# Kernel tuning notes

Measured on AMD Instinct MI355X. Metric: run time of the kernel, lower is better.

## Reference

```python
import jax, jax.numpy as jnp
import numpy as np

B, S, A = 64, 256, 256
V, P, TE, PE, AE, H, L = 50000, 48, 256, 64, 64, 512, 24
WD = TE + PE          # word_dim = token_embed + pos_embed
NA = 3 * L + 3        # Shift + L Unary + 2L Reduce/Reduce* + Pad + Pop


def setup_inputs() -> dict:
    key = jax.random.key(0)
    ks = jax.random.split(key, 24)
    f = lambda i, shape: jax.random.normal(ks[i], shape, dtype=jnp.float32) * 0.05
    return dict(
        token_batch=jax.random.randint(ks[0], (B, S), 0, V),
        pos_batch=jax.random.randint(ks[1], (B, S), 0, P),
        label_batch=jax.random.randint(ks[2], (B, S), 0, L),
        action_batch=jax.random.randint(ks[3], (B, A), 0, NA - 2),  # exclude Pad/Pop
        word_emb=f(4, (V, TE)), pos_emb=f(5, (P, PE)), action_emb=f(6, (NA, AE)),
        tok_Wih=f(7, (4 * H, WD)), tok_Whh=f(8, (4 * H, H)), tok_b=f(9, (4 * H,)),
        st_Wih=f(10, (4 * H, H)), st_Whh=f(11, (4 * H, H)), st_b=f(12, (4 * H,)),
        ac_Wih=f(13, (4 * H, AE)), ac_Whh=f(14, (4 * H, H)), ac_b=f(15, (4 * H,)),
        red_W=f(16, (2 * L, WD, 2 * WD)), red_b=f(17, (2 * L, WD)),
        comp_W=f(18, (H, WD)), comp_b=f(19, (H,)),
        h2f_W=f(20, (H, 5 * H)), h2f_b=f(21, (H,)),
        f2a_W=f(22, (NA, H)), f2a_b=f(23, (NA,)),
    )


def _lstm_cell(x, h, c, Wih, Whh, b):
    g = x @ Wih.T + h @ Whh.T + b
    i, fg, gg, o = jnp.split(g, 4, axis=-1)
    c = jax.nn.sigmoid(fg) * c + jax.nn.sigmoid(i) * jnp.tanh(gg)
    return jax.nn.sigmoid(o) * jnp.tanh(c), c


def reference(token_batch, pos_batch, label_batch, action_batch,
              word_emb, pos_emb, action_emb,
              tok_Wih, tok_Whh, tok_b,
              st_Wih, st_Whh, st_b,
              ac_Wih, ac_Whh, ac_b,
              red_W, red_b, comp_W, comp_b,
              h2f_W, h2f_b, f2a_W, f2a_b):
    # token encoder: embed + concat + unidirectional LSTM over the sentence
    tok = jnp.concatenate([word_emb[token_batch], pos_emb[pos_batch]], -1)  # [B,S,WD]

    def tstep(carry, x):
        h, c = carry
        h, c = _lstm_cell(x, h, c, tok_Wih, tok_Whh, tok_b)
        return (h, c), h

    h0 = jnp.zeros((B, H), tok.dtype)
    (_, _), tok_out = jax.lax.scan(tstep, (h0, h0), jnp.swapaxes(tok, 0, 1))  # [S,B,H]

    # action-step scan: action LSTMCell + per-label tiny linear composition +
    # stack LSTMCell + 5H decision feature -> hidden2feat -> relu -> feat2act
    a_emb = action_emb[action_batch]                      # [B,A,AE]
    labels = action_batch % (2 * L)                        # per-step label selection
    tok_prev = jnp.concatenate([tok[:, :1], tok[:, :-1]], 1)
    pair = jnp.concatenate([tok[:, :A], tok_prev[:, :A]], -1)  # [B,A,2WD]

    def astep(carry, x):
        ha, ca, hs, cs, h1 = carry
        ae_t, lab_t, pair_t, buf_t, act_t = x
        ha, ca = _lstm_cell(ae_t, ha, ca, ac_Wih, ac_Whh, ac_b)
        # per-label reduce linear (2*WD -> WD), gathered by the step's label
        composed = jnp.tanh(jnp.einsum('bij,bj->bi', red_W[lab_t], pair_t) + red_b[lab_t])
        st_in = buf_t + composed @ comp_W.T + comp_b
        hs_new, cs = _lstm_cell(st_in, hs, cs, st_Wih, st_Whh, st_b)
        feat = jnp.concatenate([hs_new, hs, h1, buf_t, ha], -1)  # [B,5H]
        logits = jax.nn.relu(feat @ h2f_W.T + h2f_b) @ f2a_W.T + f2a_b
        logp = jax.nn.log_softmax(logits, -1)
        loss_t = -jnp.take_along_axis(logp, act_t[:, None], 1)[:, 0]
        return (ha, ca, hs_new, cs, hs), loss_t

    z = jnp.zeros((B, H), tok.dtype)
    xs = (jnp.swapaxes(a_emb, 0, 1), labels.T, jnp.swapaxes(pair, 0, 1),
          tok_out[:A], action_batch.T)
    _, losses = jax.lax.scan(astep, (z, z, z, z, z), xs)  # [A,B]
    return jnp.mean(losses)
```

## Files before the change

kernel.cpp:

```cpp
#include <hip/hip_runtime.h>
#include <math.h>

constexpr int nB = 64, nS = 256, nAc = 256, nH = 512, nG = 2048;
constexpr int nWD = 320, nNA = 75, nLB = 48, nFH = 2560;
constexpr int BH = nB * nH;

typedef _Float16 h16;
typedef _Float16 h16x8 __attribute__((ext_vector_type(8)));
typedef _Float16 h16x4 __attribute__((ext_vector_type(4)));
typedef _Float16 h16x2 __attribute__((ext_vector_type(2)));
typedef float f32x4 __attribute__((ext_vector_type(4)));
typedef unsigned long long u64t;

__device__ __forceinline__ float sigf(float x) { return 1.0f / (1.0f + __expf(-x)); }

#if __has_builtin(__builtin_amdgcn_fdot2)
#define FDOT2(a, b, c) __builtin_amdgcn_fdot2((a), (b), (c), false)
#else
__device__ __forceinline__ float FDOT2(h16x2 a, h16x2 b, float c) {
    return c + (float)a[0] * (float)b[0] + (float)a[1] * (float)b[1];
}
#endif

__global__ void init_k(h16* __restrict__ hsrec, int* __restrict__ counts, int* __restrict__ fill,
                       u64t* __restrict__ hbuf, u64t* __restrict__ spbuf, u64t* __restrict__ apbuf)
{
    int i = blockIdx.x * 256 + threadIdx.x;
    if (i < 2 * BH) hsrec[i] = (h16)0.0f;
    if (i < 32768) { hbuf[i] = 0; spbuf[i] = 0; apbuf[i] = 0; }
    if (i < nLB) { counts[i] = 0; fill[i] = 0; }
}

__global__ __launch_bounds__(256)
void cvt_k(const float* __restrict__ src, h16* __restrict__ dst, int n4)
{
    const int i = blockIdx.x * 256 + threadIdx.x;
    if (i < n4) {
        const float4 a = ((const float4*)src)[i];
        h16x4 v; v[0]=(h16)a.x; v[1]=(h16)a.y; v[2]=(h16)a.z; v[3]=(h16)a.w;
        ((h16x4*)dst)[i] = v;
    }
}

__global__ __launch_bounds__(64)
void embed_k(const int* __restrict__ tokb, const int* __restrict__ posb,
             const float* __restrict__ wemb, const float* __restrict__ pemb,
             h16* __restrict__ tok)
{
    const int r = blockIdx.x;
    const int tid = threadIdx.x;
    const int tk = tokb[r], pp = posb[r];
    h16x8* d = (h16x8*)(tok + (size_t)r * nWD);
    if (tid < 32) {
        const float4* sw = (const float4*)(wemb + (size_t)tk * 256);
        const float4 a = sw[2 * tid], b = sw[2 * tid + 1];
        h16x8 o;
        o[0]=(h16)a.x; o[1]=(h16)a.y; o[2]=(h16)a.z; o[3]=(h16)a.w;
        o[4]=(h16)b.x; o[5]=(h16)b.y; o[6]=(h16)b.z; o[7]=(h16)b.w;
        d[tid] = o;
    } else if (tid < 40) {
        const int q = tid - 32;
        const float4* sp = (const float4*)(pemb + (size_t)pp * 64);
        const float4 a = sp[2 * q], b = sp[2 * q + 1];
        h16x8 o;
        o[0]=(h16)a.x; o[1]=(h16)a.y; o[2]=(h16)a.z; o[3]=(h16)a.w;
        o[4]=(h16)b.x; o[5]=(h16)b.y; o[6]=(h16)b.z; o[7]=(h16)b.w;
        d[32 + q] = o;
    }
}

__global__ __launch_bounds__(256)
void actab_k(const float* __restrict__ aemb, const float* __restrict__ aWih,
             const float* __restrict__ ab, float* __restrict__ acTab)
{
    const int a = blockIdx.x;
    __shared__ float ae[64];
    const int tid = threadIdx.x;
    if (tid < 64) ae[tid] = aemb[a * 64 + tid];
    __syncthreads();
    for (int j = tid; j < nG; j += 256) {
        const float* wr = aWih + (size_t)j * 64;
        float s = ab[j];
        #pragma unroll
        for (int k = 0; k < 64; k += 4) {
            const float4 w = *(const float4*)(wr + k);
            s = fmaf(w.x, ae[k], s);     s = fmaf(w.y, ae[k + 1], s);
            s = fmaf(w.z, ae[k + 2], s); s = fmaf(w.w, ae[k + 3], s);
        }
        acTab[(size_t)a * nG + j] = s;
    }
}

template<int MODE, bool RELU>
__global__ __launch_bounds__(256)
void mgemm_k(const h16* __restrict__ Wm, const float* __restrict__ bias,
             const h16* __restrict__ A0, const h16* __restrict__ A1,
             const h16* __restrict__ A2, h16* __restrict__ C, int Ktot, int ldC)
{
    const int bm = blockIdx.x << 6, bn = blockIdx.y << 6;
    const int tid = threadIdx.x;
    const int lane = tid & 63, wave = tid >> 6;
    const int wr = wave >> 1, wc = wave & 1;
    __shared__ __align__(16) h16 As[64][40];
    __shared__ __align__(16) h16 Ws[64][40];
    const int srow = tid >> 2, sk = (tid & 3) << 3;
    const int r3 = bm + srow;
    const h16* arow = nullptr;
    if (MODE == 0) { const int b = r3 & 63, s = r3 >> 6; arow = A0 + ((size_t)b * nS + s) * nWD; }
    if (MODE == 5) { arow = A0 + (size_t)r3 * nWD; }
    const h16* wrow = Wm + (size_t)(bn + srow) * Ktot;
    f32x4 acc[2][2] = {};
    for (int k0 = 0; k0 < Ktot; k0 += 32) {
        h16x8 av, wv;
        if (MODE == 3) {
            const int k = k0 + sk;
            const int p = k >> 9;
            const h16* base = (p == 0) ? A0 + 2 * BH : (p == 1) ? A0 + BH
                            : (p == 2) ? A0 : (p == 3) ? A1 : A2;
            av = *(const h16x8*)(base + (size_t)r3 * nH + (k & 511));
        } else {
            av = *(const h16x8*)(arow + k0 + sk);
        }
        wv = *(const h16x8*)(wrow + k0 + sk);
        __syncthreads();
        *(h16x8*)(&As[srow][sk]) = av;
        *(h16x8*)(&Ws[srow][sk]) = wv;
        __syncthreads();
        const int fk = (lane >> 4) << 3;
        const int fr = lane & 15;
        h16x8 af0 = *(const h16x8*)(&As[(wr << 5) + fr][fk]);
        h16x8 af1 = *(const h16x8*)(&As[(wr << 5) + 16 + fr][fk]);
        h16x8 bf0 = *(const h16x8*)(&Ws[(wc << 5) + fr][fk]);
        h16x8 bf1 = *(const h16x8*)(&Ws[(wc << 5) + 16 + fr][fk]);
        acc[0][0] = __builtin_amdgcn_mfma_f32_16x16x32_f16(af0, bf0, acc[0][0], 0, 0, 0);
        acc[0][1] = __builtin_amdgcn_mfma_f32_16x16x32_f16(af0, bf1, acc[0][1], 0, 0, 0);
        acc[1][0] = __builtin_amdgcn_mfma_f32_16x16x32_f16(af1, bf0, acc[1][0], 0, 0, 0);
        acc[1][1] = __builtin_amdgcn_mfma_f32_16x16x32_f16(af1, bf1, acc[1][1], 0, 0, 0);
    }
    #pragma unroll
    for (int mi = 0; mi < 2; ++mi) {
        #pragma unroll
        for (int ni = 0; ni < 2; ++ni) {
            const int col = bn + (wc << 5) + (ni << 4) + (lane & 15);
            const float bs = bias[col];
            #pragma unroll
            for (int rg = 0; rg < 4; ++rg) {
                const int row = bm + (wr << 5) + (mi << 4) + ((lane >> 4) << 2) + rg;
                float x = acc[mi][ni][rg] + bs;
                if (RELU) x = fmaxf(x, 0.0f);
                C[(size_t)row * ldC + col] = (h16)x;
            }
        }
    }
}

__global__ void hist_k(const int* __restrict__ actb, int* __restrict__ lab, int* __restrict__ counts)
{
    const int r = blockIdx.x * 256 + threadIdx.x;
    const int t = r >> 6, b = r & 63;
    const int a = actb[b * nAc + t];
    const int l = a % nLB;
    lab[r] = l;
    atomicAdd(&counts[l], 1);
}

__global__ void tiles_k(const int* __restrict__ counts, int* __restrict__ offs,
                        int* __restrict__ tl_lab, int* __restrict__ tl_start,
                        int* __restrict__ tl_cnt, int* __restrict__ ntiles)
{
    if (blockIdx.x == 0 && threadIdx.x == 0) {
        int o = 0, nt = 0;
        for (int l = 0; l < nLB; ++l) {
            offs[l] = o;
            const int c = counts[l];
            for (int s0 = 0; s0 < c; s0 += 64) {
                tl_lab[nt] = l; tl_start[nt] = o + s0; tl_cnt[nt] = min(64, c - s0); ++nt;
            }
            o += c;
        }
        offs[nLB] = o;
        ntiles[0] = nt;
    }
}

__global__ void scatter_k(const int* __restrict__ lab, const int* __restrict__ offs,
                          int* __restrict__ fill, int* __restrict__ idx)
{
    const int r = blockIdx.x * 256 + threadIdx.x;
    const int l = lab[r];
    const int pos = offs[l] + atomicAdd(&fill[l], 1);
    idx[pos] = r;
}

__global__ __launch_bounds__(256)
void comp_gemm_k(const h16* __restrict__ tok, const float* __restrict__ redW,
                 const float* __restrict__ redb, const int* __restrict__ idx,
                 const int* __restrict__ tl_lab, const int* __restrict__ tl_start,
                 const int* __restrict__ tl_cnt, const int* __restrict__ ntiles,
                 h16* __restrict__ comp)
{
    const int tile = blockIdx.x;
    if (tile >= ntiles[0]) return;
    const int cn0 = blockIdx.y << 6;
    const int l = tl_lab[tile], rst = tl_start[tile], mrows = tl_cnt[tile];
    __shared__ int rows_s[64];
    __shared__ __align__(16) float As[16][68];
    __shared__ __align__(16) float Ws[16][68];
    const int tid = threadIdx.x;
    if (tid < 64) rows_s[tid] = (tid < mrows) ? idx[rst + tid] : -1;
    __syncthreads();
    const int alm = tid >> 1, alk = (tid & 1) << 3;
    const int wlm = tid >> 2, wlk = (tid & 3) << 2;
    const int trow = tid >> 4, tcol = tid & 15;
    const int rm = (tid < 128) ? rows_s[alm] : -1;
    const h16* arow0 = tok;
    const h16* arow1 = tok;
    if (rm >= 0) {
        const int b = rm & 63, t = rm >> 6;
        arow0 = tok + ((size_t)b * nS + t) * nWD;
        arow1 = tok + ((size_t)b * nS + max(t - 1, 0)) * nWD;
    }
    const float* wrow = redW + (size_t)l * (320 * 640) + (size_t)(cn0 + wlm) * 640;
    float acc[4][4] = {};
    for (int k0 = 0; k0 < 640; k0 += 16) {
        const int k = k0 + alk;
        h16x8 av = {};
        if (rm >= 0) av = (k < 320) ? *(const h16x8*)(arow0 + k)
                                    : *(const h16x8*)(arow1 + (k - 320));
        const float4 wv = *(const float4*)(wrow + k0 + wlk);
        __syncthreads();
        if (tid < 128) {
            #pragma unroll
            for (int j = 0; j < 8; ++j) As[alk + j][alm] = (float)av[j];
        }
        Ws[wlk + 0][wlm] = wv.x; Ws[wlk + 1][wlm] = wv.y;
        Ws[wlk + 2][wlm] = wv.z; Ws[wlk + 3][wlm] = wv.w;
        __syncthreads();
        #pragma unroll
        for (int kk = 0; kk < 16; ++kk) {
            const float4 a4 = *(const float4*)&As[kk][trow << 2];
            const float4 w4 = *(const float4*)&Ws[kk][tcol << 2];
            const float aa[4] = {a4.x, a4.y, a4.z, a4.w};
            const float ww[4] = {w4.x, w4.y, w4.z, w4.w};
            #pragma unroll
            for (int i = 0; i < 4; ++i)
                #pragma unroll
                for (int j = 0; j < 4; ++j)
                    acc[i][j] = fmaf(aa[i], ww[j], acc[i][j]);
        }
    }
    #pragma unroll
    for (int i = 0; i < 4; ++i) {
        const int rr = rows_s[(trow << 2) + i];
        if (rr < 0) continue;
        #pragma unroll
        for (int j = 0; j < 4; ++j) {
            const int cc = cn0 + (tcol << 2) + j;
            comp[(size_t)rr * nWD + cc] = (h16)tanhf(acc[i][j] + redb[l * nWD + cc]);
        }
    }
}

__global__ __launch_bounds__(512, 4)
void fused_scan_k(const h16* __restrict__ tW16, const h16* __restrict__ sWhh16,
                  const h16* __restrict__ sWih16, const h16* __restrict__ aW16,
                  const h16* __restrict__ gxTok, const float* __restrict__ acTab,
                  const int* __restrict__ actb, const h16* __restrict__ P1h,
                  const float* __restrict__ sbias,
                  u64t* __restrict__ hq_tok, u64t* __restrict__ hq_st, u64t* __restrict__ hq_ac,
                  h16* __restrict__ tokrec, h16* __restrict__ hsrec, h16* __restrict__ harec)
{
    __shared__ __align__(16) h16 hsmS[8][nH];
    __shared__ __align__(16) h16 hsmT[8][nH];
    __shared__ float psF[4096];
    __shared__ float gexF[1152];
    __shared__ int aidx[8];
    const int blk = blockIdx.x;
    const int tid = threadIdx.x;

    if (blk < 256) {
        const int role = blk >> 7;
        const int sub = blk & 127;
        const int g = sub >> 4, jb = sub & 15;
        const int kg = tid >> 7;
        const int r = tid & 127;
        const int c = r >> 5, jl = r & 31;
        const int grow = c * nH + (jb << 5) + jl;
        const h16* W = role ? aW16 : tW16;
        u64t* hq = role ? hq_ac : hq_tok;
        h16x8 wreg[16];
        {
            const h16* wp = W + (size_t)grow * nH + (kg << 7);
            #pragma unroll
            for (int i = 0; i < 16; ++i) wreg[i] = *(const h16x8*)(wp + (i << 3));
        }
        float creg[2] = {0.0f, 0.0f};
        const size_t gbase = (size_t)g << 11;
        for (int t = 0; t < nS; ++t) {
            float gp[2];
            if (role == 0) {
                #pragma unroll
                for (int u = 0; u < 2; ++u)
                    gp[u] = (float)gxTok[(size_t)((t << 6) + (g << 3) + (kg << 1) + u) * nG + grow];
            } else if (tid < 8) {
                aidx[tid] = actb[((g << 3) + tid) * nAc + t];
            }
            if (t == 0) {
                ((uint4*)hsmS)[tid] = make_uint4(0u, 0u, 0u, 0u);
            } else {
                const int want = t;
                u64t* base = hq + (size_t)((t - 1) & 1) * 16384 + gbase;
                u64t v[4];
                #pragma unroll
                for (int i = 0; i < 4; ++i)
                    v[i] = __hip_atomic_load(base + tid + (i << 9), __ATOMIC_RELAXED, __HIP_MEMORY_SCOPE_AGENT);
                #pragma unroll
                for (int i = 0; i < 4; ++i) {
                    while ((int)(v[i] >> 32) != want) {
                        __builtin_amdgcn_s_sleep(1);
                        v[i] = __hip_atomic_load(base + tid + (i << 9), __ATOMIC_RELAXED, __HIP_MEMORY_SCOPE_AGENT);
                    }
                    ((unsigned*)hsmS)[tid + (i << 9)] = (unsigned)v[i];
                }
            }
            __syncthreads();
            if (role == 1) {
                #pragma unroll
                for (int u = 0; u < 2; ++u)
                    gp[u] = acTab[(size_t)aidx[(kg << 1) + u] * nG + grow];
            }
            float acc[8] = {0,0,0,0,0,0,0,0};
            #pragma unroll
            for (int i = 0; i < 16; ++i) {
                const h16x2* wp = (const h16x2*)&wreg[i];
                #pragma unroll
                for (int b = 0; b < 8; ++b) {
                    h16x8 hv = *(const h16x8*)(&hsmS[b][(kg << 7) + (i << 3)]);
                    const h16x2* hp = (const h16x2*)&hv;
                    acc[b] = FDOT2(hp[0], wp[0], acc[b]);
                    acc[b] = FDOT2(hp[1], wp[1], acc[b]);
                    acc[b] = FDOT2(hp[2], wp[2], acc[b]);
                    acc[b] = FDOT2(hp[3], wp[3], acc[b]);
                }
            }
            #pragma unroll
            for (int b = 0; b < 8; ++b) psF[(((kg << 3) + b) << 7) + r] = acc[b];
            __syncthreads();
            #pragma unroll
            for (int u = 0; u < 2; ++u) {
                const int b = (kg << 1) + u;
                float s = gp[u];
                #pragma unroll
                for (int k2 = 0; k2 < 4; ++k2) s += psF[(((k2 << 3) + b) << 7) + r];
                gexF[r * 9 + b] = s;
            }
            if (role == 0 && t >= 2 && tid == 0) {
                u64t* fp = hq_st + (size_t)(t & 1) * 16384 + gbase;
                u64t v = __hip_atomic_load(fp, __ATOMIC_RELAXED, __HIP_MEMORY_SCOPE_AGENT);
                while ((int)(v >> 32) < t - 1) {
                    __builtin_amdgcn_s_sleep(1);
                    v = __hip_atomic_load(fp, __ATOMIC_RELAXED, __HIP_MEMORY_SCOPE_AGENT);
                }
            }
            __syncthreads();
            if (tid < 128) {
                const int q = tid >> 3, b2 = tid & 7;
                const int jl0 = q << 1;
                float hn[2];
                #pragma unroll
                for (int u = 0; u < 2; ++u) {
                    const int j = jl0 + u;
                    const float gi = gexF[j * 9 + b2], gf = gexF[(32 + j) * 9 + b2];
                    const float gg = gexF[(64 + j) * 9 + b2], go = gexF[(96 + j) * 9 + b2];
                    const float cn = sigf(gf) * creg[u] + sigf(gi) * tanhf(gg);
                    hn[u] = sigf(go) * tanhf(cn);
                    creg[u] = cn;
                }
                const int bg = (g << 3) + b2;
                h16x2 hp2; hp2[0] = (h16)hn[0]; hp2[1] = (h16)hn[1];
                const u64t word = ((u64t)(unsigned)(t + 1) << 32) | __builtin_bit_cast(unsigned, hp2);
                __hip_atomic_store(hq + (size_t)(t & 1) * 16384 + ((size_t)bg << 8) + (jb << 4) + q,
                                   word, __ATOMIC_RELAXED, __HIP_MEMORY_SCOPE_AGENT);
                h16* rec = role ? (harec + (size_t)t * BH) : (tokrec + (size_t)t * BH);
                *(h16x2*)(rec + (size_t)bg * nH + (jb << 5) + jl0) = hp2;
            }
        }
    } else {
        const int sub = blk - 256;
        const int g = sub >> 5, jb = sub & 31;
        const int kg = tid >> 6;
        const int r = tid & 63;
        const int c = r >> 4, jl = r & 15;
        const int grow = c * nH + (jb << 4) + jl;
        h16x8 wregA[8], wregB[8];
        {
            const h16* wa = sWhh16 + (size_t)grow * nH + (kg << 6);
            const h16* wb = sWih16 + (size_t)grow * nH + (kg << 6);
            #pragma unroll
            for (int i = 0; i < 8; ++i) {
                wregA[i] = *(const h16x8*)(wa + (i << 3));
                wregB[i] = *(const h16x8*)(wb + (i << 3));
            }
        }
        const float gbias = sbias[grow];
        float creg[2] = {0.0f, 0.0f};
        const size_t gbase = (size_t)g << 11;
        for (int t = 0; t < nAc; ++t) {
            if (t == 0) {
                ((uint4*)hsmS)[tid] = make_uint4(0u, 0u, 0u, 0u);
            } else {
                const int want = t;
                u64t* base = hq_st + (size_t)((t - 1) & 1) * 16384 + gbase;
                u64t v[4];
                #pragma unroll
                for (int i = 0; i < 4; ++i)
                    v[i] = __hip_atomic_load(base + tid + (i << 9), __ATOMIC_RELAXED, __HIP_MEMORY_SCOPE_AGENT);
                #pragma unroll
                for (int i = 0; i < 4; ++i) {
                    while ((int)(v[i] >> 32) != want) {
                        __builtin_amdgcn_s_sleep(1);
                        v[i] = __hip_atomic_load(base + tid + (i << 9), __ATOMIC_RELAXED, __HIP_MEMORY_SCOPE_AGENT);
                    }
                    ((unsigned*)hsmS)[tid + (i << 9)] = (unsigned)v[i];
                }
            }
            {
                const int want = t + 1;
                u64t* base = hq_tok + (size_t)(t & 1) * 16384 + gbase;
                const unsigned* p1p = (const unsigned*)(P1h + (size_t)t * BH) + (g << 11);
                u64t v[4];
                #pragma unroll
                for (int i = 0; i < 4; ++i)
                    v[i] = __hip_atomic_load(base + tid + (i << 9), __ATOMIC_RELAXED, __HIP_MEMORY_SCOPE_AGENT);
                #pragma unroll
                for (int i = 0; i < 4; ++i) {
                    while ((int)(v[i] >> 32) != want) {
                        __builtin_amdgcn_s_sleep(1);
                        v[i] = __hip_atomic_load(base + tid + (i << 9), __ATOMIC_RELAXED, __HIP_MEMORY_SCOPE_AGENT);
                    }
                    const h16x2 tv = __builtin_bit_cast(h16x2, (unsigned)v[i]);
                    const h16x2 pv = __builtin_bit_cast(h16x2, p1p[tid + (i << 9)]);
                    h16x2 sum; sum[0] = tv[0] + pv[0]; sum[1] = tv[1] + pv[1];
                    ((unsigned*)hsmT)[tid + (i << 9)] = __builtin_bit_cast(unsigned, sum);
                }
            }
            __syncthreads();
            float acc[8] = {0,0,0,0,0,0,0,0};
            #pragma unroll
            for (int i = 0; i < 8; ++i) {
                const h16x2* wa = (const h16x2*)&wregA[i];
                const h16x2* wb = (const h16x2*)&wregB[i];
                #pragma unroll
                for (int b = 0; b < 8; ++b) {
                    h16x8 hs = *(const h16x8*)(&hsmS[b][(kg << 6) + (i << 3)]);
                    h16x8 ht = *(const h16x8*)(&hsmT[b][(kg << 6) + (i << 3)]);
                    const h16x2* hps = (const h16x2*)&hs;
                    const h16x2* hpt = (const h16x2*)&ht;
                    #pragma unroll
                    for (int p = 0; p < 4; ++p) {
                        acc[b] = FDOT2(hps[p], wa[p], acc[b]);
                        acc[b] = FDOT2(hpt[p], wb[p], acc[b]);
                    }
                }
            }
            #pragma unroll
            for (int b = 0; b < 8; ++b) psF[(((kg << 3) + b) << 6) + r] = acc[b];
            __syncthreads();
            {
                const int b = kg;
                float s = gbias;
                #pragma unroll
                for (int k2 = 0; k2 < 8; ++k2) s += psF[(((k2 << 3) + b) << 6) + r];
                gexF[r * 9 + b] = s;
            }
            __syncthreads();
            if (tid < 64) {
                const int q = tid >> 3, b2 = tid & 7;
                const int jl0 = q << 1;
                float hn[2];
                #pragma unroll
                for (int u = 0; u < 2; ++u) {
                    const int j = jl0 + u;
                    const float gi = gexF[j * 9 + b2], gf = gexF[(16 + j) * 9 + b2];
                    const float gg = gexF[(32 + j) * 9 + b2], go = gexF[(48 + j) * 9 + b2];
                    const float cn = sigf(gf) * creg[u] + sigf(gi) * tanhf(gg);
                    hn[u] = sigf(go) * tanhf(cn);
                    creg[u] = cn;
                }
                const int bg = (g << 3) + b2;
                h16x2 hp2; hp2[0] = (h16)hn[0]; hp2[1] = (h16)hn[1];
                const u64t word = ((u64t)(unsigned)(t + 1) << 32) | __builtin_bit_cast(unsigned, hp2);
                __hip_atomic_store(hq_st + (size_t)(t & 1) * 16384 + ((size_t)bg << 8) + (jb << 3) + q,
                                   word, __ATOMIC_RELAXED, __HIP_MEMORY_SCOPE_AGENT);
                *(h16x2*)(hsrec + (size_t)(t + 2) * BH + (size_t)bg * nH + (jb << 4) + jl0) = hp2;
            }
        }
    }
}

__global__ __launch_bounds__(128)
void loss_k(const h16* __restrict__ hidden, const float* __restrict__ f2aW,
            const float* __restrict__ f2ab, const int* __restrict__ actb,
            float* __restrict__ losses)
{
    const int r = blockIdx.x;
    const int t = r >> 6, b = r & 63;
    __shared__ __align__(16) float hrow[nH];
    __shared__ float lg[nNA + 1];
    const int tid = threadIdx.x;
    if (tid < 64) {
        const h16x8 v = ((const h16x8*)(hidden + (size_t)r * nH))[tid];
        #pragma unroll
        for (int j = 0; j < 8; ++j) hrow[tid * 8 + j] = (float)v[j];
    }
    __syncthreads();
    if (tid < nNA) {
        const float* wr = f2aW + (size_t)tid * nH;
        float a = f2ab[tid];
        for (int k = 0; k < nH; k += 4) {
            const float4 wv = *(const float4*)(wr + k);
            const float4 hv = *(const float4*)(&hrow[k]);
            a = fmaf(wv.x, hv.x, a); a = fmaf(wv.y, hv.y, a);
            a = fmaf(wv.z, hv.z, a); a = fmaf(wv.w, hv.w, a);
        }
        lg[tid] = a;
    }
    __syncthreads();
    if (tid < 64) {
        float m = -1e30f;
        for (int i = tid; i < nNA; i += 64) m = fmaxf(m, lg[i]);
        #pragma unroll
        for (int o = 32; o > 0; o >>= 1) m = fmaxf(m, __shfl_xor(m, o));
        float s = 0.0f;
        for (int i = tid; i < nNA; i += 64) s += __expf(lg[i] - m);
        #pragma unroll
        for (int o = 32; o > 0; o >>= 1) s += __shfl_xor(s, o);
        if (tid == 0) {
            const int a = actb[b * nAc + t];
            losses[r] = m + logf(s) - lg[a];
        }
    }
}

__global__ __launch_bounds__(256)
void reduce_k(const float* __restrict__ losses, float* __restrict__ out)
{
    __shared__ float sm[256];
    const int tid = threadIdx.x;
    float a = 0.0f;
    for (int i = tid; i < nS * nB; i += 256) a += losses[i];
    sm[tid] = a; __syncthreads();
    for (int s = 128; s > 0; s >>= 1) { if (tid < s) sm[tid] += sm[tid + s]; __syncthreads(); }
    if (tid == 0) out[0] = sm[0] * (1.0f / 16384.0f);
}

extern "C" void kernel_launch(void* const* d_in, const int* in_sizes, int n_in,
                              void* d_out, int out_size, void* d_ws, size_t ws_size,
                              hipStream_t stream)
{
    const int*   tokb  = (const int*)  d_in[0];
    const int*   posb  = (const int*)  d_in[1];
    const int*   actb  = (const int*)  d_in[3];
    const float* wemb  = (const float*)d_in[4];
    const float* pemb  = (const float*)d_in[5];
    const float* aemb  = (const float*)d_in[6];
    const float* tWih  = (const float*)d_in[7];
    const float* tWhh  = (const float*)d_in[8];
    const float* tb    = (const float*)d_in[9];
    const float* sWih  = (const float*)d_in[10];
    const float* sWhh  = (const float*)d_in[11];
    const float* sb    = (const float*)d_in[12];
    const float* aWih  = (const float*)d_in[13];
    const float* aWhh  = (const float*)d_in[14];
    const float* ab    = (const float*)d_in[15];
    const float* redW  = (const float*)d_in[16];
    const float* redb  = (const float*)d_in[17];
    const float* compW = (const float*)d_in[18];
    const float* compb = (const float*)d_in[19];
    const float* h2fW  = (const float*)d_in[20];
    const float* h2fb  = (const float*)d_in[21];
    const float* f2aW  = (const float*)d_in[22];
    const float* f2ab  = (const float*)d_in[23];

    char* base = (char*)d_ws;
    auto carve = [&](size_t bytes) { char* p = base; base += (bytes + 255) & ~(size_t)255; return p; };
    h16*   tok    = (h16*)  carve((size_t)nB * nS * nWD * 2);
    h16*   Xh     = (h16*)  carve((size_t)nS * nB * nG * 2);
    h16*   comph  = (h16*)  carve((size_t)nS * nB * nWD * 2);
    h16*   P1h    = (h16*)  carve((size_t)nS * BH * 2);
    h16*   tokrec = (h16*)  carve((size_t)nS * BH * 2);
    h16*   hsrec  = (h16*)  carve((size_t)(nS + 2) * BH * 2);
    h16*   harec  = (h16*)  carve((size_t)nS * BH * 2);
    h16*   tW16   = (h16*)  carve((size_t)nG * nH * 2);
    h16*   sW16   = (h16*)  carve((size_t)nG * nH * 2);
    h16*   aW16   = (h16*)  carve((size_t)nG * nH * 2);
    h16*   tWih16 = (h16*)  carve((size_t)nG * nWD * 2);
    h16*   sWih16 = (h16*)  carve((size_t)nG * nH * 2);
    h16*   h2f16  = (h16*)  carve((size_t)nH * nFH * 2);
    h16*   comp16 = (h16*)  carve((size_t)nH * nWD * 2);
    float* acTab  = (float*)carve((size_t)nNA * nG * 4);
    u64t*  hbuf   = (u64t*) carve((size_t)2 * 16384 * 8);
    u64t*  spbuf  = (u64t*) carve((size_t)2 * 16384 * 8);
    u64t*  apbuf  = (u64t*) carve((size_t)2 * 16384 * 8);
    float* losses = (float*)carve((size_t)nS * nB * 4);
    int*   lab      = (int*)carve((size_t)nS * nB * 4);
    int*   counts   = (int*)carve(nLB * 4);
    int*   offs     = (int*)carve((nLB + 1) * 4);
    int*   fill     = (int*)carve(nLB * 4);
    int*   tl_lab   = (int*)carve(320 * 4);
    int*   tl_start = (int*)carve(320 * 4);
    int*   tl_cnt   = (int*)carve(320 * 4);
    int*   ntiles   = (int*)carve(4);
    int*   idxb     = (int*)carve((size_t)nS * nB * 4);

    init_k<<<dim3(256), dim3(256), 0, stream>>>(hsrec, counts, fill, hbuf, spbuf, apbuf);
    embed_k<<<dim3(nB * nS), dim3(64), 0, stream>>>(tokb, posb, wemb, pemb, tok);
    actab_k<<<dim3(nNA), dim3(256), 0, stream>>>(aemb, aWih, ab, acTab);
    cvt_k<<<dim3(1024), dim3(256), 0, stream>>>(tWhh, tW16, 262144);
    cvt_k<<<dim3(1024), dim3(256), 0, stream>>>(sWhh, sW16, 262144);
    cvt_k<<<dim3(1024), dim3(256), 0, stream>>>(aWhh, aW16, 262144);
    cvt_k<<<dim3(640),  dim3(256), 0, stream>>>(tWih, tWih16, 163840);
    cvt_k<<<dim3(1024), dim3(256), 0, stream>>>(sWih, sWih16, 262144);
    cvt_k<<<dim3(1280), dim3(256), 0, stream>>>(h2fW, h2f16, 327680);
    cvt_k<<<dim3(160),  dim3(256), 0, stream>>>(compW, comp16, 40960);
    mgemm_k<0,false><<<dim3(256, 32), dim3(256), 0, stream>>>(tWih16, tb, tok, nullptr, nullptr, Xh, nWD, nG);
    hist_k<<<dim3(64), dim3(256), 0, stream>>>(actb, lab, counts);
    tiles_k<<<dim3(1), dim3(64), 0, stream>>>(counts, offs, tl_lab, tl_start, tl_cnt, ntiles);
    scatter_k<<<dim3(64), dim3(256), 0, stream>>>(lab, offs, fill, idxb);
    comp_gemm_k<<<dim3(304, 5), dim3(256), 0, stream>>>(tok, redW, redb, idxb, tl_lab, tl_start, tl_cnt, ntiles, comph);
    mgemm_k<5,false><<<dim3(256, 8), dim3(256), 0, stream>>>(comp16, compb, comph, nullptr, nullptr, P1h, nWD, nH);
    {
        const h16* a0 = tW16; const h16* a1 = sW16; const h16* a2 = sWih16; const h16* a3 = aW16;
        const h16* a4 = Xh; const float* a5 = acTab; const int* a6 = actb;
        const h16* a7 = P1h; const float* a8 = sb;
        u64t* a9 = hbuf; u64t* a10 = spbuf; u64t* a11 = apbuf;
        h16* a12 = tokrec; h16* a13 = hsrec; h16* a14 = harec;
        void* args[] = {&a0, &a1, &a2, &a3, &a4, &a5, &a6, &a7, &a8, &a9, &a10, &a11, &a12, &a13, &a14};
        hipLaunchCooperativeKernel((const void*)fused_scan_k, dim3(512), dim3(512), args, 0, stream);
    }
    mgemm_k<3,true><<<dim3(256, 8), dim3(256), 0, stream>>>(h2f16, h2fb, hsrec, tokrec, harec, Xh, nFH, nH);
    loss_k<<<dim3(nS * nB), dim3(128), 0, stream>>>(Xh, f2aW, f2ab, actb, losses);
    reduce_k<<<dim3(1), dim3(256), 0, stream>>>(losses, (float*)d_out);
}
```

Before: 3.177 ms.

## Split stack LSTM input projection into separate pipelined role ahead of recurrence

The persistent cooperative scan kernel is reorganised into four 256-block roles: token LSTM, action LSTM, a stack-input projection (sWih times token output plus P1) and the stack recurrence (sWhh). The input projection for step t is computed ahead and passed through an 8-deep flagged ring buffer, so the serial stack recurrence only does one 512-wide matvec per step instead of two. Token outputs are also forwarded through a 4-deep ring, with backpressure waits widened accordingly. Blocks shrink to 256 threads with 1024 blocks, and scheduling priority is raised around the dot-product loop. The cost is more inter-block flag traffic and larger sync buffers, with deadlock risk if not all 1024 blocks are co-resident.

Result: slower. 3.876 ms (+22.0%).

```diff
diff --git a/kernel.cpp b/kernel.cpp
--- a/kernel.cpp
+++ b/kernel.cpp
@@ -22,12 +22,18 @@
 }
 #endif
 
+#define PINV(x) asm volatile("" : "+v"(x))
+
 __global__ void init_k(h16* __restrict__ hsrec, int* __restrict__ counts, int* __restrict__ fill,
-                       u64t* __restrict__ hbuf, u64t* __restrict__ spbuf, u64t* __restrict__ apbuf)
+                       u64t* __restrict__ hbuf, u64t* __restrict__ spbuf, u64t* __restrict__ apbuf,
+                       u64t* __restrict__ tsbuf, u64t* __restrict__ x2buf)
 {
     int i = blockIdx.x * 256 + threadIdx.x;
     if (i < 2 * BH) hsrec[i] = (h16)0.0f;
     if (i < 32768) { hbuf[i] = 0; spbuf[i] = 0; apbuf[i] = 0; }
+    tsbuf[i] = 0;
+    #pragma unroll
+    for (int j = 0; j < 8; ++j) x2buf[(size_t)j * 65536 + i] = 0;
     if (i < nLB) { counts[i] = 0; fill[i] = 0; }
 }
 
@@ -261,239 +267,183 @@
     }
 }
 
-__global__ __launch_bounds__(512, 4)
+__global__ __launch_bounds__(256, 4)
 void fused_scan_k(const h16* __restrict__ tW16, const h16* __restrict__ sWhh16,
                   const h16* __restrict__ sWih16, const h16* __restrict__ aW16,
                   const h16* __restrict__ gxTok, const float* __restrict__ acTab,
                   const int* __restrict__ actb, const h16* __restrict__ P1h,
                   const float* __restrict__ sbias,
                   u64t* __restrict__ hq_tok, u64t* __restrict__ hq_st, u64t* __restrict__ hq_ac,
+                  u64t* __restrict__ hq_ts, u64t* __restrict__ hq_x2,
                   h16* __restrict__ tokrec, h16* __restrict__ hsrec, h16* __restrict__ harec)
 {
     __shared__ __align__(16) h16 hsmS[8][nH];
-    __shared__ __align__(16) h16 hsmT[8][nH];
-    __shared__ float psF[4096];
-    __shared__ float gexF[1152];
+    __shared__ float ps[4][8][65];
+    __shared__ float gexF[64 * 9];
     __shared__ int aidx[8];
-    const int blk = blockIdx.x;
-    const int tid = threadIdx.x;
-
-    if (blk < 256) {
-        const int role = blk >> 7;
-        const int sub = blk & 127;
-        const int g = sub >> 4, jb = sub & 15;
-        const int kg = tid >> 7;
-        const int r = tid & 127;
-        const int c = r >> 5, jl = r & 31;
-        const int grow = c * nH + (jb << 5) + jl;
-        const h16* W = role ? aW16 : tW16;
-        u64t* hq = role ? hq_ac : hq_tok;
-        h16x8 wreg[16];
-        {
-            const h16* wp = W + (size_t)grow * nH + (kg << 7);
-            #pragma unroll
-            for (int i = 0; i < 16; ++i) wreg[i] = *(const h16x8*)(wp + (i << 3));
-        }
-        float creg[2] = {0.0f, 0.0f};
-        const size_t gbase = (size_t)g << 11;
-        for (int t = 0; t < nS; ++t) {
-            float gp[2];
-            if (role == 0) {
-                #pragma unroll
-                for (int u = 0; u < 2; ++u)
-                    gp[u] = (float)gxTok[(size_t)((t << 6) + (g << 3) + (kg << 1) + u) * nG + grow];
-            } else if (tid < 8) {
-                aidx[tid] = actb[((g << 3) + tid) * nAc + t];
-            }
-            if (t == 0) {
-                ((uint4*)hsmS)[tid] = make_uint4(0u, 0u, 0u, 0u);
-            } else {
-                const int want = t;
-                u64t* base = hq + (size_t)((t - 1) & 1) * 16384 + gbase;
-                u64t v[4];
-                #pragma unroll
-                for (int i = 0; i < 4; ++i)
-                    v[i] = __hip_atomic_load(base + tid + (i << 9), __ATOMIC_RELAXED, __HIP_MEMORY_SCOPE_AGENT);
-                #pragma unroll
-                for (int i = 0; i < 4; ++i) {
-                    while ((int)(v[i] >> 32) != want) {
-                        __builtin_amdgcn_s_sleep(1);
-                        v[i] = __hip_atomic_load(base + tid + (i << 9), __ATOMIC_RELAXED, __HIP_MEMORY_SCOPE_AGENT);
-                    }
-                    ((unsigned*)hsmS)[tid + (i << 9)] = (unsigned)v[i];
+    const int blk = blockIdx.x, tid = threadIdx.x;
+    const int role = blk >> 8, sub = blk & 255;
+    const int g = sub & 7, jb = sub >> 3;
+    const int kg = tid & 3, r = tid >> 2;
+    const int grow = (r >> 4) * nH + (jb << 4) + (r & 15);
+    const int rr = tid & 63, bq = tid >> 6;
+    const int growR = (rr >> 4) * nH + (jb << 4) + (rr & 15);
+    const size_t gbase = (size_t)g << 11;
+    const h16* W = (role == 0) ? tW16 : (role == 1) ? aW16 : (role == 2) ? sWih16 : sWhh16;
+    u64t* hq_self = (role == 0) ? hq_tok : (role == 1) ? hq_ac : hq_st;
+    h16x8 wreg[16];
+    {
+        const h16* Wp = W + (size_t)grow * nH;
+        #pragma unroll
+        for (int i = 0; i < 16; ++i) wreg[i] = *(const h16x8*)(Wp + (((i << 2) + kg) << 3));
+        #pragma unroll
+        for (int i = 0; i < 16; ++i) PINV(wreg[i]);
+    }
+    const float sxb = (role == 2) ? sbias[growR] : 0.0f;
+    float creg[2] = {0.0f, 0.0f};
+    for (int t = 0; t < nS; ++t) {
+        float gp[2] = {0.0f, 0.0f};
+        if (role == 0) {
+            #pragma unroll
+            for (int u = 0; u < 2; ++u)
+                gp[u] = (float)gxTok[(size_t)((t << 6) + (g << 3) + (bq << 1) + u) * nG + growR];
+        } else if (role == 1 && tid < 8) {
+            aidx[tid] = actb[((g << 3) + tid) * nAc + t];
+        }
+        if (role == 2) {
+            const int want = t + 1;
+            u64t* base = hq_ts + (size_t)(t & 3) * 16384 + gbase;
+            const unsigned* p1p = (const unsigned*)(P1h + (size_t)t * BH) + (g << 11);
+            u64t v[8];
+            #pragma unroll
+            for (int i = 0; i < 8; ++i)
+                v[i] = __hip_atomic_load(base + tid + (i << 8), __ATOMIC_RELAXED, __HIP_MEMORY_SCOPE_AGENT);
+            #pragma unroll
+            for (int i = 0; i < 8; ++i) {
+                while ((int)(v[i] >> 32) != want) {
+                    __builtin_amdgcn_s_sleep(1);
+                    v[i] = __hip_atomic_load(base + tid + (i << 8), __ATOMIC_RELAXED, __HIP_MEMORY_SCOPE_AGENT);
                 }
-            }
-            __syncthreads();
-            if (role == 1) {
-                #pragma unroll
-                for (int u = 0; u < 2; ++u)
-                    gp[u] = acTab[(size_t)aidx[(kg << 1) + u] * nG + grow];
-            }
-            float acc[8] = {0,0,0,0,0,0,0,0};
-            #pragma unroll
-            for (int i = 0; i < 16; ++i) {
-                const h16x2* wp = (const h16x2*)&wreg[i];
-                #pragma unroll
-                for (int b = 0; b < 8; ++b) {
-                    h16x8 hv = *(const h16x8*)(&hsmS[b][(kg << 7) + (i << 3)]);
-                    const h16x2* hp = (const h16x2*)&hv;
-                    acc[b] = FDOT2(hp[0], wp[0], acc[b]);
-                    acc[b] = FDOT2(hp[1], wp[1], acc[b]);
-                    acc[b] = FDOT2(hp[2], wp[2], acc[b]);
-                    acc[b] = FDOT2(hp[3], wp[3], acc[b]);
+                const h16x2 tv = __builtin_bit_cast(h16x2, (unsigned)v[i]);
+                const h16x2 pv = __builtin_bit_cast(h16x2, p1p[tid + (i << 8)]);
+                h16x2 sum; sum[0] = tv[0] + pv[0]; sum[1] = tv[1] + pv[1];
+                ((unsigned*)hsmS)[tid + (i << 8)] = __builtin_bit_cast(unsigned, sum);
+            }
+        } else if (t == 0) {
+            #pragma unroll
+            for (int i = 0; i < 8; ++i) ((unsigned*)hsmS)[tid + (i << 8)] = 0u;
+        } else {
+            const int want = t;
+            u64t* base = hq_self + (size_t)((t - 1) & 1) * 16384 + gbase;
+            u64t v[8];
+            #pragma unroll
+            for (int i = 0; i < 8; ++i)
+                v[i] = __hip_atomic_load(base + tid + (i << 8), __ATOMIC_RELAXED, __HIP_MEMORY_SCOPE_AGENT);
+            #pragma unroll
+            for (int i = 0; i < 8; ++i) {
+                while ((int)(v[i] >> 32) != want) {
+                    __builtin_amdgcn_s_sleep(1);
+                    v[i] = __hip_atomic_load(base + tid + (i << 8), __ATOMIC_RELAXED, __HIP_MEMORY_SCOPE_AGENT);
                 }
-            }
-            #pragma unroll
-            for (int b = 0; b < 8; ++b) psF[(((kg << 3) + b) << 7) + r] = acc[b];
-            __syncthreads();
+                ((unsigned*)hsmS)[tid + (i << 8)] = (unsigned)v[i];
+            }
+        }
+        __syncthreads();
+        if (role == 1) {
+            #pragma unroll
+            for (int u = 0; u < 2; ++u)
+                gp[u] = acTab[(size_t)aidx[(bq << 1) + u] * nG + growR];
+        }
+        __builtin_amdgcn_s_setprio(1);
+        float acc[8] = {0,0,0,0,0,0,0,0};
+        #pragma unroll
+        for (int i = 0; i < 16; ++i) {
+            const h16x2* wp = (const h16x2*)&wreg[i];
+            const int ko = ((i << 2) + kg) << 3;
+            #pragma unroll
+            for (int b = 0; b < 8; ++b) {
+                h16x8 hv = *(const h16x8*)(&hsmS[b][ko]);
+                const h16x2* hp = (const h16x2*)&hv;
+                acc[b] = FDOT2(hp[0], wp[0], acc[b]);
+                acc[b] = FDOT2(hp[1], wp[1], acc[b]);
+                acc[b] = FDOT2(hp[2], wp[2], acc[b]);
+                acc[b] = FDOT2(hp[3], wp[3], acc[b]);
+            }
+        }
+        __builtin_amdgcn_s_setprio(0);
+        #pragma unroll
+        for (int b = 0; b < 8; ++b) ps[kg][b][r] = acc[b];
+        __syncthreads();
+        #pragma unroll
+        for (int u = 0; u < 2; ++u) {
+            const int b = (bq << 1) + u;
+            float s = (role == 2) ? sxb : gp[u];
+            #pragma unroll
+            for (int k2 = 0; k2 < 4; ++k2) s += ps[k2][b][rr];
+            if (role == 3) {
+                const int want = t + 1;
+                u64t* xp = hq_x2 + (size_t)(t & 7) * 65536 + ((size_t)g << 13) + (b << 10) + (jb << 5) + (rr >> 1);
+                u64t v = __hip_atomic_load(xp, __ATOMIC_RELAXED, __HIP_MEMORY_SCOPE_AGENT);
+                while ((int)(v >> 32) != want) {
+                    __builtin_amdgcn_s_sleep(1);
+                    v = __hip_atomic_load(xp, __ATOMIC_RELAXED, __HIP_MEMORY_SCOPE_AGENT);
+                }
+                const h16x2 xv = __builtin_bit_cast(h16x2, (unsigned)v);
+                s += (float)xv[rr & 1];
+            }
+            gexF[rr * 9 + b] = s;
+        }
+        if (role == 0 && t >= 4 && tid == 0) {
+            u64t* fp = hq_x2 + (size_t)((t - 4) & 7) * 65536 + ((size_t)g << 13);
+            u64t v = __hip_atomic_load(fp, __ATOMIC_RELAXED, __HIP_MEMORY_SCOPE_AGENT);
+            while ((int)(v >> 32) < t - 3) {
+                __builtin_amdgcn_s_sleep(1);
+                v = __hip_atomic_load(fp, __ATOMIC_RELAXED, __HIP_MEMORY_SCOPE_AGENT);
+            }
+        }
+        if (role == 2 && t >= 8 && tid == 0) {
+            u64t* fp = hq_st + (size_t)(t & 1) * 16384 + gbase;
+            u64t v = __hip_atomic_load(fp, __ATOMIC_RELAXED, __HIP_MEMORY_SCOPE_AGENT);
+            while ((int)(v >> 32) < t - 7) {
+                __builtin_amdgcn_s_sleep(1);
+                v = __hip_atomic_load(fp, __ATOMIC_RELAXED, __HIP_MEMORY_SCOPE_AGENT);
+            }
+        }
+        __syncthreads();
+        if (role == 2) {
+            const int rp = tid >> 3, b2 = tid & 7;
+            const float v0 = gexF[(rp << 1) * 9 + b2];
+            const float v1 = gexF[((rp << 1) + 1) * 9 + b2];
+            h16x2 p; p[0] = (h16)v0; p[1] = (h16)v1;
+            const u64t word = ((u64t)(unsigned)(t + 1) << 32) | __builtin_bit_cast(unsigned, p);
+            __hip_atomic_store(hq_x2 + (size_t)(t & 7) * 65536 + ((size_t)g << 13) + (b2 << 10) + (jb << 5) + rp,
+                               word, __ATOMIC_RELAXED, __HIP_MEMORY_SCOPE_AGENT);
+        } else if (tid < 64) {
+            const int qp = tid >> 3, b2 = tid & 7;
+            const int j0 = qp << 1;
+            float hn[2];
             #pragma unroll
             for (int u = 0; u < 2; ++u) {
-                const int b = (kg << 1) + u;
-                float s = gp[u];
-                #pragma unroll
-                for (int k2 = 0; k2 < 4; ++k2) s += psF[(((k2 << 3) + b) << 7) + r];
-                gexF[r * 9 + b] = s;
-            }
-            if (role == 0 && t >= 2 && tid == 0) {
-                u64t* fp = hq_st + (size_t)(t & 1) * 16384 + gbase;
-                u64t v = __hip_atomic_load(fp, __ATOMIC_RELAXED, __HIP_MEMORY_SCOPE_AGENT);
-                while ((int)(v >> 32) < t - 1) {
-                    __builtin_amdgcn_s_sleep(1);
-                    v = __hip_atomic_load(fp, __ATOMIC_RELAXED, __HIP_MEMORY_SCOPE_AGENT);
-                }
-            }
-            __syncthreads();
-            if (tid < 128) {
-                const int q = tid >> 3, b2 = tid & 7;
-                const int jl0 = q << 1;
-                float hn[2];
-                #pragma unroll
-                for (int u = 0; u < 2; ++u) {
-                    const int j = jl0 + u;
-                    const float gi = gexF[j * 9 + b2], gf = gexF[(32 + j) * 9 + b2];
-                    const float gg = gexF[(64 + j) * 9 + b2], go = gexF[(96 + j) * 9 + b2];
-                    const float cn = sigf(gf) * creg[u] + sigf(gi) * tanhf(gg);
-                    hn[u] = sigf(go) * tanhf(cn);
-                    creg[u] = cn;
-                }
-                const int bg = (g << 3) + b2;
-                h16x2 hp2; hp2[0] = (h16)hn[0]; hp2[1] = (h16)hn[1];
-                const u64t word = ((u64t)(unsigned)(t + 1) << 32) | __builtin_bit_cast(unsigned, hp2);
-                __hip_atomic_store(hq + (size_t)(t & 1) * 16384 + ((size_t)bg << 8) + (jb << 4) + q,
+                const int j = j0 + u;
+                const float gi = gexF[j * 9 + b2], gf = gexF[(16 + j) * 9 + b2];
+                const float gg = gexF[(32 + j) * 9 + b2], go = gexF[(48 + j) * 9 + b2];
+                const float cn = sigf(gf) * creg[u] + sigf(gi) * tanhf(gg);
+                hn[u] = sigf(go) * tanhf(cn);
+                creg[u] = cn;
+            }
+            const int bg = (g << 3) + b2;
+            h16x2 hp2; hp2[0] = (h16)hn[0]; hp2[1] = (h16)hn[1];
+            const u64t word = ((u64t)(unsigned)(t + 1) << 32) | __builtin_bit_cast(unsigned, hp2);
+            const size_t woff = ((size_t)b2 << 8) + (jb << 3) + qp;
+            __hip_atomic_store(hq_self + (size_t)(t & 1) * 16384 + gbase + woff,
+                               word, __ATOMIC_RELAXED, __HIP_MEMORY_SCOPE_AGENT);
+            if (role == 0)
+                __hip_atomic_store(hq_ts + (size_t)(t & 3) * 16384 + gbase + woff,
                                    word, __ATOMIC_RELAXED, __HIP_MEMORY_SCOPE_AGENT);
-                h16* rec = role ? (harec + (size_t)t * BH) : (tokrec + (size_t)t * BH);
-                *(h16x2*)(rec + (size_t)bg * nH + (jb << 5) + jl0) = hp2;
-            }
-        }
-    } else {
-        const int sub = blk - 256;
-        const int g = sub >> 5, jb = sub & 31;
-        const int kg = tid >> 6;
-        const int r = tid & 63;
-        const int c = r >> 4, jl = r & 15;
-        const int grow = c * nH + (jb << 4) + jl;
-        h16x8 wregA[8], wregB[8];
-        {
-            const h16* wa = sWhh16 + (size_t)grow * nH + (kg << 6);
-            const h16* wb = sWih16 + (size_t)grow * nH + (kg << 6);
-            #pragma unroll
-            for (int i = 0; i < 8; ++i) {
-                wregA[i] = *(const h16x8*)(wa + (i << 3));
-                wregB[i] = *(const h16x8*)(wb + (i << 3));
-            }
-        }
-        const float gbias = sbias[grow];
-        float creg[2] = {0.0f, 0.0f};
-        const size_t gbase = (size_t)g << 11;
-        for (int t = 0; t < nAc; ++t) {
-            if (t == 0) {
-                ((uint4*)hsmS)[tid] = make_uint4(0u, 0u, 0u, 0u);
-            } else {
-                const int want = t;
-                u64t* base = hq_st + (size_t)((t - 1) & 1) * 16384 + gbase;
-                u64t v[4];
-                #pragma unroll
-                for (int i = 0; i < 4; ++i)
-                    v[i] = __hip_atomic_load(base + tid + (i << 9), __ATOMIC_RELAXED, __HIP_MEMORY_SCOPE_AGENT);
-                #pragma unroll
-                for (int i = 0; i < 4; ++i) {
-                    while ((int)(v[i] >> 32) != want) {
-                        __builtin_amdgcn_s_sleep(1);
-                        v[i] = __hip_atomic_load(base + tid + (i << 9), __ATOMIC_RELAXED, __HIP_MEMORY_SCOPE_AGENT);
-                    }
-                    ((unsigned*)hsmS)[tid + (i << 9)] = (unsigned)v[i];
-                }
-            }
-            {
-                const int want = t + 1;
-                u64t* base = hq_tok + (size_t)(t & 1) * 16384 + gbase;
-                const unsigned* p1p = (const unsigned*)(P1h + (size_t)t * BH) + (g << 11);
-                u64t v[4];
-                #pragma unroll
-                for (int i = 0; i < 4; ++i)
-                    v[i] = __hip_atomic_load(base + tid + (i << 9), __ATOMIC_RELAXED, __HIP_MEMORY_SCOPE_AGENT);
-                #pragma unroll
-                for (int i = 0; i < 4; ++i) {
-                    while ((int)(v[i] >> 32) != want) {
-                        __builtin_amdgcn_s_sleep(1);
-                        v[i] = __hip_atomic_load(base + tid + (i << 9), __ATOMIC_RELAXED, __HIP_MEMORY_SCOPE_AGENT);
-                    }
-                    const h16x2 tv = __builtin_bit_cast(h16x2, (unsigned)v[i]);
-                    const h16x2 pv = __builtin_bit_cast(h16x2, p1p[tid + (i << 9)]);
-                    h16x2 sum; sum[0] = tv[0] + pv[0]; sum[1] = tv[1] + pv[1];
-                    ((unsigned*)hsmT)[tid + (i << 9)] = __builtin_bit_cast(unsigned, sum);
-                }
-            }
-            __syncthreads();
-            float acc[8] = {0,0,0,0,0,0,0,0};
-            #pragma unroll
-            for (int i = 0; i < 8; ++i) {
-                const h16x2* wa = (const h16x2*)&wregA[i];
-                const h16x2* wb = (const h16x2*)&wregB[i];
-                #pragma unroll
-                for (int b = 0; b < 8; ++b) {
-                    h16x8 hs = *(const h16x8*)(&hsmS[b][(kg << 6) + (i << 3)]);
-                    h16x8 ht = *(const h16x8*)(&hsmT[b][(kg << 6) + (i << 3)]);
-                    const h16x2* hps = (const h16x2*)&hs;
-                    const h16x2* hpt = (const h16x2*)&ht;
-                    #pragma unroll
-                    for (int p = 0; p < 4; ++p) {
-                        acc[b] = FDOT2(hps[p], wa[p], acc[b]);
-                        acc[b] = FDOT2(hpt[p], wb[p], acc[b]);
-                    }
-                }
-            }
-            #pragma unroll
-            for (int b = 0; b < 8; ++b) psF[(((kg << 3) + b) << 6) + r] = acc[b];
-            __syncthreads();
-            {
-                const int b = kg;
-                float s = gbias;
-                #pragma unroll
-                for (int k2 = 0; k2 < 8; ++k2) s += psF[(((k2 << 3) + b) << 6) + r];
-                gexF[r * 9 + b] = s;
-            }
-            __syncthreads();
-            if (tid < 64) {
-                const int q = tid >> 3, b2 = tid & 7;
-                const int jl0 = q << 1;
-                float hn[2];
-                #pragma unroll
-                for (int u = 0; u < 2; ++u) {
-                    const int j = jl0 + u;
-                    const float gi = gexF[j * 9 + b2], gf = gexF[(16 + j) * 9 + b2];
-                    const float gg = gexF[(32 + j) * 9 + b2], go = gexF[(48 + j) * 9 + b2];
-                    const float cn = sigf(gf) * creg[u] + sigf(gi) * tanhf(gg);
-                    hn[u] = sigf(go) * tanhf(cn);
-                    creg[u] = cn;
-                }
-                const int bg = (g << 3) + b2;
-                h16x2 hp2; hp2[0] = (h16)hn[0]; hp2[1] = (h16)hn[1];
-                const u64t word = ((u64t)(unsigned)(t + 1) << 32) | __builtin_bit_cast(unsigned, hp2);
-                __hip_atomic_store(hq_st + (size_t)(t & 1) * 16384 + ((size_t)bg << 8) + (jb << 3) + q,
-                                   word, __ATOMIC_RELAXED, __HIP_MEMORY_SCOPE_AGENT);
-                *(h16x2*)(hsrec + (size_t)(t + 2) * BH + (size_t)bg * nH + (jb << 4) + jl0) = hp2;
-            }
+            h16* rec = (role == 0) ? (tokrec + (size_t)t * BH)
+                     : (role == 1) ? (harec + (size_t)t * BH)
+                                   : (hsrec + (size_t)(t + 2) * BH);
+            *(h16x2*)(rec + (size_t)bg * nH + (jb << 4) + j0) = hp2;
         }
     }
 }
@@ -602,6 +552,8 @@
     u64t*  hbuf   = (u64t*) carve((size_t)2 * 16384 * 8);
     u64t*  spbuf  = (u64t*) carve((size_t)2 * 16384 * 8);
     u64t*  apbuf  = (u64t*) carve((size_t)2 * 16384 * 8);
+    u64t*  tsbuf  = (u64t*) carve((size_t)4 * 16384 * 8);
+    u64t*  x2buf  = (u64t*) carve((size_t)8 * 65536 * 8);
     float* losses = (float*)carve((size_t)nS * nB * 4);
     int*   lab      = (int*)carve((size_t)nS * nB * 4);
     int*   counts   = (int*)carve(nLB * 4);
@@ -613,7 +565,7 @@
     int*   ntiles   = (int*)carve(4);
     int*   idxb     = (int*)carve((size_t)nS * nB * 4);
 
-    init_k<<<dim3(256), dim3(256), 0, stream>>>(hsrec, counts, fill, hbuf, spbuf, apbuf);
+    init_k<<<dim3(256), dim3(256), 0, stream>>>(hsrec, counts, fill, hbuf, spbuf, apbuf, tsbuf, x2buf);
     embed_k<<<dim3(nB * nS), dim3(64), 0, stream>>>(tokb, posb, wemb, pemb, tok);
     actab_k<<<dim3(nNA), dim3(256), 0, stream>>>(aemb, aWih, ab, acTab);
     cvt_k<<<dim3(1024), dim3(256), 0, stream>>>(tWhh, tW16, 262144);
@@ -633,10 +585,10 @@
         const h16* a0 = tW16; const h16* a1 = sW16; const h16* a2 = sWih16; const h16* a3 = aW16;
         const h16* a4 = Xh; const float* a5 = acTab; const int* a6 = actb;
         const h16* a7 = P1h; const float* a8 = sb;
-        u64t* a9 = hbuf; u64t* a10 = spbuf; u64t* a11 = apbuf;
-        h16* a12 = tokrec; h16* a13 = hsrec; h16* a14 = harec;
-        void* args[] = {&a0, &a1, &a2, &a3, &a4, &a5, &a6, &a7, &a8, &a9, &a10, &a11, &a12, &a13, &a14};
-        hipLaunchCooperativeKernel((const void*)fused_scan_k, dim3(512), dim3(512), args, 0, stream);
+        u64t* a9 = hbuf; u64t* a10 = spbuf; u64t* a11 = apbuf; u64t* a12 = tsbuf; u64t* a13 = x2buf;
+        h16* a14 = tokrec; h16* a15 = hsrec; h16* a16 = harec;
+        void* args[] = {&a0, &a1, &a2, &a3, &a4, &a5, &a6, &a7, &a8, &a9, &a10, &a11, &a12, &a13, &a14, &a15, &a16};
+        hipLaunchCooperativeKernel((const void*)fused_scan_k, dim3(1024), dim3(256), args, 0, stream);
     }
     mgemm_k<3,true><<<dim3(256, 8), dim3(256), 0, stream>>>(h2f16, h2fb, hsrec, tokrec, harec, Xh, nFH, nH);
     loss_k<<<dim3(nS * nB), dim3(128), 0, stream>>>(Xh, f2aW, f2ab, actb, losses);
```
